# Kernel tuning notes

Measured on AMD Instinct MI355X. Metric: run time of the kernel, lower is better.

The kernel has to match this reference:

```python
import jax, jax.numpy as jnp
import numpy as np

EMBED_DIM = 2048
NUM_HEADS = 16
HEAD_DIM = EMBED_DIM // NUM_HEADS
BASE = 10000.0


def rotate_half(x):
    half = x.shape[-1] // 2
    x1, x2 = x[..., :half], x[..., half:]
    return jnp.concatenate([-x2, x1], axis=-1)


def apply_rope(x, base=BASE):
    # x: [B, H, S, Dh]
    S, Dh = x.shape[-2], x.shape[-1]
    inv_freq = 1.0 / (base ** (jnp.arange(0, Dh, 2, dtype=jnp.float32) / Dh))
    t = jnp.arange(S, dtype=jnp.float32)
    freqs = jnp.einsum('i,j->ij', t, inv_freq)          # [S, Dh/2]
    emb = jnp.concatenate([freqs, freqs], axis=-1)      # [S, Dh]
    return x * jnp.cos(emb) + rotate_half(x) * jnp.sin(emb)


def setup_inputs() -> dict:
    key = jax.random.key(0)
    ks = jax.random.split(key, 9)
    B, S, D = 2, 2048, EMBED_DIM
    xavier = lambda k, shape: jax.random.uniform(
        k, shape, jnp.float32, -1.0, 1.0) * float(np.sqrt(6.0 / (shape[0] + shape[1])))
    return {
        'x': jax.random.normal(ks[0], (B, S, D), jnp.float32),
        'q_w': xavier(ks[1], (D, D)),
        'k_w': xavier(ks[2], (D, D)),
        'v_w': xavier(ks[3], (D, D)),
        'q_b': jnp.zeros((D,), jnp.float32),
        'k_b': jnp.zeros((D,), jnp.float32),
        'v_b': jnp.zeros((D,), jnp.float32),
        'out_w': xavier(ks[4], (D, D)),
        'out_b': jnp.zeros((D,), jnp.float32),
    }


def reference(x, q_w, k_w, v_w, q_b, k_b, v_b, out_w, out_b):
    B, S, D = x.shape
    H, Dh = NUM_HEADS, HEAD_DIM
    scaling = Dh ** -0.5
    # F.linear(x, W, b) = x @ W.T + b
    q = (x @ q_w.T + q_b).reshape(B, S, H, Dh).transpose(0, 2, 1, 3)
    k = (x @ k_w.T + k_b).reshape(B, S, H, Dh).transpose(0, 2, 1, 3)
    v = (x @ v_w.T + v_b).reshape(B, S, H, Dh).transpose(0, 2, 1, 3)
    q = apply_rope(q)
    k = apply_rope(k)
    attn = jnp.einsum('bhqd,bhkd->bhqk', q, k) * scaling
    probs = jax.nn.softmax(attn, axis=-1)
    out = jnp.einsum('bhqk,bhkd->bhqd', probs, v)
    out = out.transpose(0, 2, 1, 3).reshape(B, S, D)
    return out @ out_w.T + out_b
```

## Files before the change

### kernel.cpp

```cpp
#include <hip/hip_runtime.h>
#include <stdint.h>

typedef __bf16 bf16;
typedef __bf16 bf16x4 __attribute__((ext_vector_type(4)));
typedef __bf16 bf16x8 __attribute__((ext_vector_type(8)));
typedef float f32x4 __attribute__((ext_vector_type(4)));

#define DM 2048
#define MM 4096
#define MFMA16(a, b, c) __builtin_amdgcn_mfma_f32_16x16x32_bf16(a, b, c, 0, 0, 0)

__device__ __forceinline__ void gload_lds16(const void* g, void* l) {
  __builtin_amdgcn_global_load_lds((const __attribute__((address_space(1))) uint32_t*)g,
                                   (__attribute__((address_space(3))) uint32_t*)l, 16, 0, 0);
}

__global__ __launch_bounds__(256) void cvt_f32_bf16(
    const float* __restrict__ s0, const float* __restrict__ s1,
    const float* __restrict__ s2, const float* __restrict__ s3,
    const float* __restrict__ s4,
    bf16* __restrict__ d0, bf16* __restrict__ d1, bf16* __restrict__ d2,
    bf16* __restrict__ d3, bf16* __restrict__ d4)
{
  const size_t i4 = (size_t)(blockIdx.x * 256 + threadIdx.x) * 4;
  const float* s; bf16* d; size_t off;
  if      (i4 <  8388608u) { s = s0; d = d0; off = i4;             }
  else if (i4 < 12582912u) { s = s1; d = d1; off = i4 -  8388608u; }
  else if (i4 < 16777216u) { s = s2; d = d2; off = i4 - 12582912u; }
  else if (i4 < 20971520u) { s = s3; d = d3; off = i4 - 16777216u; }
  else                     { s = s4; d = d4; off = i4 - 20971520u; }
  const float4 v = *(const float4*)(s + off);
  bf16x4 o = { (bf16)v.x, (bf16)v.y, (bf16)v.z, (bf16)v.w };
  *(bf16x4*)(d + off) = o;
}

__global__ __launch_bounds__(256, 2) void gemm_qkv_fused(
    const bf16* __restrict__ A,
    const bf16* __restrict__ Wq, const bf16* __restrict__ Wk, const bf16* __restrict__ Wv,
    const float* __restrict__ qb, const float* __restrict__ kb, const float* __restrict__ vb,
    bf16* __restrict__ Cq, bf16* __restrict__ Ck, bf16* __restrict__ Cv)
{
  __shared__ __align__(16) bf16 As[128 * 32];
  __shared__ __align__(16) bf16 Ws[3 * 128 * 32];
  const int id = blockIdx.x;
  const int xcd = id & 7, jj = id >> 3;
  const int n0 = (xcd * 2 + (jj >> 5)) * 128;
  const int m0 = (jj & 31) * 128;

  const int t = threadIdx.x;
  const int wave = t >> 6, lane = t & 63;
  const int quad = lane >> 4, c16 = lane & 15;
  const int wr = wave >> 1, wc = wave & 1;

  f32x4 acc[3][4][4] = {};

  const int rowA = t >> 2;
  const int colA = (t & 3) * 8;
  const bf16* gA  = A  + (size_t)(m0 + rowA) * DM + colA;
  const bf16* gW0 = Wq + (size_t)(n0 + rowA) * DM + colA;
  const bf16* gW1 = Wk + (size_t)(n0 + rowA) * DM + colA;
  const bf16* gW2 = Wv + (size_t)(n0 + rowA) * DM + colA;
  bf16* lA  = As + wave * 512;
  bf16* lW0 = Ws + wave * 512;
  bf16* lW1 = Ws + 4096 + wave * 512;
  bf16* lW2 = Ws + 8192 + wave * 512;

  for (int k0 = 0; k0 < DM; k0 += 32) {
    gload_lds16(gA,  lA);
    gload_lds16(gA  + (size_t)64 * DM, lA  + 2048);
    gload_lds16(gW0, lW0);
    gload_lds16(gW0 + (size_t)64 * DM, lW0 + 2048);
    gload_lds16(gW1, lW1);
    gload_lds16(gW1 + (size_t)64 * DM, lW1 + 2048);
    gload_lds16(gW2, lW2);
    gload_lds16(gW2 + (size_t)64 * DM, lW2 + 2048);
    gA += 32; gW0 += 32; gW1 += 32; gW2 += 32;
    __syncthreads();

    bf16x8 af[4];
#pragma unroll
    for (int i = 0; i < 4; ++i)
      af[i] = *(const bf16x8*)&As[(wr * 64 + i * 16 + c16) * 32 + quad * 8];
#pragma unroll
    for (int z = 0; z < 3; ++z) {
      bf16x8 bfr[4];
#pragma unroll
      for (int jx = 0; jx < 4; ++jx)
        bfr[jx] = *(const bf16x8*)&Ws[z * 4096 + (wc * 64 + jx * 16 + c16) * 32 + quad * 8];
#pragma unroll
      for (int i = 0; i < 4; ++i)
#pragma unroll
        for (int jx = 0; jx < 4; ++jx)
          acc[z][i][jx] = MFMA16(af[i], bfr[jx], acc[z][i][jx]);
    }
    __syncthreads();
  }

#pragma unroll
  for (int z = 0; z < 2; ++z) {
    bf16* C = (z == 0) ? Cq : Ck;
    const float* bias = (z == 0) ? qb : kb;
#pragma unroll
    for (int jx = 0; jx < 4; ++jx) {
      const int col = n0 + wc * 64 + jx * 16 + c16;
      const float bv = bias[col];
#pragma unroll
      for (int i = 0; i < 4; ++i) {
        const int row = m0 + wr * 64 + i * 16 + quad * 4;
#pragma unroll
        for (int r = 0; r < 4; ++r)
          C[(size_t)(row + r) * DM + col] = (bf16)(acc[z][i][jx][r] + bv);
      }
    }
  }
  {
    const int h = n0 >> 7;
#pragma unroll
    for (int jx = 0; jx < 4; ++jx) {
      const int d = wc * 64 + jx * 16 + c16;
      const float bv = vb[n0 + d];
#pragma unroll
      for (int i = 0; i < 4; ++i) {
        const int row = m0 + wr * 64 + i * 16 + quad * 4;
        const int b = row >> 11, s = row & 2047;
        bf16x4 o;
#pragma unroll
        for (int r = 0; r < 4; ++r) o[r] = (bf16)(acc[2][i][jx][r] + bv);
        *(bf16x4*)&Cv[((size_t)((b * 16 + h) * 128 + d)) * 2048 + s] = o;
      }
    }
  }
}

__global__ __launch_bounds__(256) void gemm_bias_f32(
    const bf16* __restrict__ A, const bf16* __restrict__ W,
    const float* __restrict__ bias, float* __restrict__ C)
{
  __shared__ __align__(16) bf16 As[128 * 32];
  __shared__ __align__(16) bf16 Bs[128 * 32];
  const int id = blockIdx.x;
  const int xcd = id & 7, jj = id >> 3;
  const int n0 = (xcd * 2 + (jj >> 5)) * 128;
  const int m0 = (jj & 31) * 128;

  const int t = threadIdx.x;
  const int wave = t >> 6, lane = t & 63;
  const int quad = lane >> 4, c16 = lane & 15;
  const int wr = wave >> 1, wc = wave & 1;

  f32x4 acc[4][4] = {};
  const int rowA = t >> 2;
  const int colA = (t & 3) * 8;
  const bf16* gA = A + (size_t)(m0 + rowA) * DM + colA;
  const bf16* gB = W + (size_t)(n0 + rowA) * DM + colA;
  bf16* lA = As + wave * 512;
  bf16* lB = Bs + wave * 512;

  for (int k0 = 0; k0 < DM; k0 += 32) {
    gload_lds16(gA, lA);
    gload_lds16(gA + (size_t)64 * DM, lA + 2048);
    gload_lds16(gB, lB);
    gload_lds16(gB + (size_t)64 * DM, lB + 2048);
    gA += 32; gB += 32;
    __syncthreads();

    bf16x8 af[4], bfr[4];
#pragma unroll
    for (int i = 0; i < 4; ++i)
      af[i] = *(const bf16x8*)&As[(wr * 64 + i * 16 + c16) * 32 + quad * 8];
#pragma unroll
    for (int jx = 0; jx < 4; ++jx)
      bfr[jx] = *(const bf16x8*)&Bs[(wc * 64 + jx * 16 + c16) * 32 + quad * 8];
#pragma unroll
    for (int i = 0; i < 4; ++i)
#pragma unroll
      for (int jx = 0; jx < 4; ++jx)
        acc[i][jx] = MFMA16(af[i], bfr[jx], acc[i][jx]);
    __syncthreads();
  }

#pragma unroll
  for (int jx = 0; jx < 4; ++jx) {
    const int col = n0 + wc * 64 + jx * 16 + c16;
    const float bv = bias[col];
#pragma unroll
    for (int i = 0; i < 4; ++i) {
      const int row = m0 + wr * 64 + i * 16 + quad * 4;
#pragma unroll
      for (int r = 0; r < 4; ++r)
        C[(size_t)(row + r) * DM + col] = acc[i][jx][r] + bv;
    }
  }
}

__global__ __launch_bounds__(256) void rope_scale(bf16* __restrict__ Q, bf16* __restrict__ K)
{
  const int idx = blockIdx.x * 256 + threadIdx.x;
  const int i = idx & 63;
  const int h = (idx >> 6) & 15;
  const int s = (idx >> 10) & 2047;
  const int b = idx >> 21;
  const size_t base = ((size_t)(b * 2048 + s)) * 2048 + (size_t)h * 128;
  const float inv_freq = __expf((float)i * -0.14391156514261228f);
  float sn, cs;
  __sincosf((float)s * inv_freq, &sn, &cs);
  const float scale = 0.08838834764831845f * 1.4426950408889634f;
  const float q1 = (float)Q[base + i], q2 = (float)Q[base + i + 64];
  Q[base + i]      = (bf16)((q1 * cs - q2 * sn) * scale);
  Q[base + i + 64] = (bf16)((q2 * cs + q1 * sn) * scale);
  const float k1 = (float)K[base + i], k2 = (float)K[base + i + 64];
  K[base + i]      = (bf16)(k1 * cs - k2 * sn);
  K[base + i + 64] = (bf16)(k2 * cs + k1 * sn);
}

__global__ __launch_bounds__(256, 2) void attn(
    const bf16* __restrict__ Q, const bf16* __restrict__ K,
    const bf16* __restrict__ Vt, bf16* __restrict__ O)
{
  __shared__ __align__(16) bf16 Ks[4][64][32];
  __shared__ __align__(16) bf16 Vs[2][128][32];
  __shared__ __align__(16) bf16 Ps[4][2][16][88];
  const int t = threadIdx.x;
  const int wave = t >> 6, lane = t & 63;
  const int quad = lane >> 4, c16 = lane & 15;
  const int id = blockIdx.x;
  const int xcd = id & 7, jj = id >> 3;
  const int bh = xcd * 4 + (jj >> 4);
  const int q0 = (jj & 15) * 128;
  const int b = bh >> 4, h = bh & 15;

  bf16x8 qf[2][4];
#pragma unroll
  for (int g = 0; g < 2; ++g) {
    const bf16* qrow = Q + (size_t)(b * 2048 + q0 + wave * 32 + g * 16 + c16) * 2048
                         + (size_t)h * 128 + quad * 8;
#pragma unroll
    for (int ks = 0; ks < 4; ++ks) qf[g][ks] = *(const bf16x8*)(qrow + ks * 32);
  }

  float l_i[2] = {0.f, 0.f};
  f32x4 o_acc[2][8] = {};

  const bf16* Kg = K + (size_t)(b * 2048) * 2048 + (size_t)h * 128;
  const bf16* Vg = Vt + (size_t)bh * 128 * 2048;

  for (int kt = 0; kt < 32; ++kt) {
    const int kt0 = kt * 64;
#pragma unroll
    for (int rr = 0; rr < 4; ++rr) {
      const int s = rr * 256 + t;
      const int ks = s >> 8, krow = (s >> 2) & 63, c8 = s & 3;
      gload_lds16(Kg + (size_t)(kt0 + krow) * 2048 + ks * 32 + c8 * 8,
                  (bf16*)Ks + (size_t)(rr * 256 + wave * 64) * 8);
    }
#pragma unroll
    for (int rr = 0; rr < 4; ++rr) {
      const int s = rr * 256 + t;
      const int kc = s >> 9, d = (s >> 2) & 127, c8 = s & 3;
      gload_lds16(Vg + (size_t)d * 2048 + kt0 + kc * 32 + c8 * 8,
                  (bf16*)Vs + (size_t)(rr * 256 + wave * 64) * 8);
    }
    __syncthreads();

    f32x4 st[2][4] = {};
#pragma unroll
    for (int ks = 0; ks < 4; ++ks)
#pragma unroll
      for (int nt = 0; nt < 4; ++nt) {
        bf16x8 kf = *(const bf16x8*)&Ks[ks][nt * 16 + c16][quad * 8];
        st[0][nt] = MFMA16(kf, qf[0][ks], st[0][nt]);
        st[1][nt] = MFMA16(kf, qf[1][ks], st[1][nt]);
      }

#pragma unroll
    for (int g = 0; g < 2; ++g) {
      float ps = 0.f;
#pragma unroll
      for (int nt = 0; nt < 4; ++nt) {
        bf16x4 pk;
#pragma unroll
        for (int r = 0; r < 4; ++r) {
          const float p = exp2f(st[g][nt][r]);
          ps += p;
          pk[r] = (bf16)p;
        }
        *(bf16x4*)&Ps[wave][g][c16][nt * 16 + quad * 4] = pk;
      }
      l_i[g] += ps;
    }

#pragma unroll
    for (int kc = 0; kc < 2; ++kc) {
      bf16x8 pf0 = *(const bf16x8*)&Ps[wave][0][c16][kc * 32 + quad * 8];
      bf16x8 pf1 = *(const bf16x8*)&Ps[wave][1][c16][kc * 32 + quad * 8];
#pragma unroll
      for (int dt = 0; dt < 8; ++dt) {
        bf16x8 vf = *(const bf16x8*)&Vs[kc][dt * 16 + c16][quad * 8];
        o_acc[0][dt] = MFMA16(vf, pf0, o_acc[0][dt]);
        o_acc[1][dt] = MFMA16(vf, pf1, o_acc[1][dt]);
      }
    }
    __syncthreads();
  }

#pragma unroll
  for (int g = 0; g < 2; ++g) {
    float l = l_i[g];
    l += __shfl_xor(l, 16, 64);
    l += __shfl_xor(l, 32, 64);
    const float invl = 1.0f / l;
    const int qrow = q0 + wave * 32 + g * 16 + c16;
    bf16* orow = O + (size_t)(b * 2048 + qrow) * 2048 + (size_t)h * 128 + quad * 4;
#pragma unroll
    for (int dt = 0; dt < 8; ++dt) {
      bf16x4 o;
#pragma unroll
      for (int r = 0; r < 4; ++r) o[r] = (bf16)(o_acc[g][dt][r] * invl);
      *(bf16x4*)(orow + dt * 16) = o;
    }
  }
}

extern "C" void kernel_launch(void* const* d_in, const int* in_sizes, int n_in,
                              void* d_out, int out_size, void* d_ws, size_t ws_size,
                              hipStream_t stream)
{
  (void)in_sizes; (void)n_in; (void)out_size; (void)ws_size;
  const float* x   = (const float*)d_in[0];
  const float* q_w = (const float*)d_in[1];
  const float* k_w = (const float*)d_in[2];
  const float* v_w = (const float*)d_in[3];
  const float* q_b = (const float*)d_in[4];
  const float* k_b = (const float*)d_in[5];
  const float* v_b = (const float*)d_in[6];
  const float* o_w = (const float*)d_in[7];
  const float* o_b = (const float*)d_in[8];

  const size_t NELEM = (size_t)MM * DM;
  const size_t WELEM = (size_t)DM * DM;
  bf16* Xb  = (bf16*)d_ws;
  bf16* Wq  = Xb + NELEM;
  bf16* Wk  = Wq + WELEM;
  bf16* Wv  = Wk + WELEM;
  bf16* Wo  = Wv + WELEM;
  bf16* Q   = Wo + WELEM;
  bf16* Kb  = Q  + NELEM;
  bf16* Vt  = Kb + NELEM;
  bf16* attnO = Xb;

  cvt_f32_bf16<<<24576, 256, 0, stream>>>(x, q_w, k_w, v_w, o_w, Xb, Wq, Wk, Wv, Wo);

  gemm_qkv_fused<<<512, 256, 0, stream>>>(Xb, Wq, Wk, Wv, q_b, k_b, v_b, Q, Kb, Vt);
  rope_scale<<<16384, 256, 0, stream>>>(Q, Kb);
  attn<<<512, 256, 0, stream>>>(Q, Kb, Vt, attnO);
  gemm_bias_f32<<<512, 256, 0, stream>>>(attnO, Wo, o_b, (float*)d_out);
}
```

Measured before the change: 410.8 us.

## Fuse RoPE into QKV GEMM epilogue, widen K-tile with XOR-swizzled LDS

Removes the separate rope_scale kernel and applies rotary embedding plus softmax scaling inside the QKV GEMM epilogue. The epilogue stages each Q/K tile through LDS so it can write coalesced 16-byte rows. Both GEMMs now load 64-wide K tiles into an XOR-swizzled LDS layout, which halves the barrier count and avoids bank conflicts. The attention kernel's launch bounds go to 3 blocks per CU with a smaller P padding, and the output GEMM gets a 2-block occupancy hint. The QKV kernel now uses 64KB of LDS, which may cut its occupancy.

```diff
diff --git a/kernel.cpp b/kernel.cpp
--- a/kernel.cpp
+++ b/kernel.cpp
@@ -40,8 +40,10 @@
     const float* __restrict__ qb, const float* __restrict__ kb, const float* __restrict__ vb,
     bf16* __restrict__ Cq, bf16* __restrict__ Ck, bf16* __restrict__ Cv)
 {
-  __shared__ __align__(16) bf16 As[128 * 32];
-  __shared__ __align__(16) bf16 Ws[3 * 128 * 32];
+  __shared__ __align__(16) bf16 smem[32768];
+  bf16* As = smem;
+  bf16* Ws = smem + 8192;
+
   const int id = blockIdx.x;
   const int xcd = id & 7, jj = id >> 3;
   const int n0 = (xcd * 2 + (jj >> 5)) * 128;
@@ -54,90 +56,118 @@
 
   f32x4 acc[3][4][4] = {};
 
-  const int rowA = t >> 2;
-  const int colA = (t & 3) * 8;
-  const bf16* gA  = A  + (size_t)(m0 + rowA) * DM + colA;
-  const bf16* gW0 = Wq + (size_t)(n0 + rowA) * DM + colA;
-  const bf16* gW1 = Wk + (size_t)(n0 + rowA) * DM + colA;
-  const bf16* gW2 = Wv + (size_t)(n0 + rowA) * DM + colA;
-  bf16* lA  = As + wave * 512;
-  bf16* lW0 = Ws + wave * 512;
-  bf16* lW1 = Ws + 4096 + wave * 512;
-  bf16* lW2 = Ws + 8192 + wave * 512;
-
-  for (int k0 = 0; k0 < DM; k0 += 32) {
-    gload_lds16(gA,  lA);
-    gload_lds16(gA  + (size_t)64 * DM, lA  + 2048);
-    gload_lds16(gW0, lW0);
-    gload_lds16(gW0 + (size_t)64 * DM, lW0 + 2048);
-    gload_lds16(gW1, lW1);
-    gload_lds16(gW1 + (size_t)64 * DM, lW1 + 2048);
-    gload_lds16(gW2, lW2);
-    gload_lds16(gW2 + (size_t)64 * DM, lW2 + 2048);
-    gA += 32; gW0 += 32; gW1 += 32; gW2 += 32;
-    __syncthreads();
-
-    bf16x8 af[4];
-#pragma unroll
-    for (int i = 0; i < 4; ++i)
-      af[i] = *(const bf16x8*)&As[(wr * 64 + i * 16 + c16) * 32 + quad * 8];
-#pragma unroll
-    for (int z = 0; z < 3; ++z) {
-      bf16x8 bfr[4];
-#pragma unroll
-      for (int jx = 0; jx < 4; ++jx)
-        bfr[jx] = *(const bf16x8*)&Ws[z * 4096 + (wc * 64 + jx * 16 + c16) * 32 + quad * 8];
-#pragma unroll
-      for (int i = 0; i < 4; ++i)
-#pragma unroll
-        for (int jx = 0; jx < 4; ++jx)
-          acc[z][i][jx] = MFMA16(af[i], bfr[jx], acc[z][i][jx]);
-    }
-    __syncthreads();
-  }
-
+  const int srow = t >> 3;
+  const int scol = ((t & 7) ^ (srow & 7)) * 8;
+  const bf16* gA  = A  + (size_t)(m0 + srow) * DM + scol;
+  const bf16* gW0 = Wq + (size_t)(n0 + srow) * DM + scol;
+  const bf16* gW1 = Wk + (size_t)(n0 + srow) * DM + scol;
+  const bf16* gW2 = Wv + (size_t)(n0 + srow) * DM + scol;
+
+  for (int k0 = 0; k0 < DM; k0 += 64) {
+#pragma unroll
+    for (int rr = 0; rr < 4; ++rr) {
+      const size_t go = (size_t)(rr * 32) * DM;
+      const int lo = (rr * 256 + wave * 64) * 8;
+      gload_lds16(gA  + go, As + lo);
+      gload_lds16(gW0 + go, Ws + lo);
+      gload_lds16(gW1 + go, Ws + 8192 + lo);
+      gload_lds16(gW2 + go, Ws + 16384 + lo);
+    }
+    gA += 64; gW0 += 64; gW1 += 64; gW2 += 64;
+    __syncthreads();
+
+#pragma unroll
+    for (int ks = 0; ks < 2; ++ks) {
+      bf16x8 af[4];
+#pragma unroll
+      for (int i = 0; i < 4; ++i) {
+        const int row = wr * 64 + i * 16 + c16;
+        const int gi = (ks * 4 + quad) ^ (row & 7);
+        af[i] = *(const bf16x8*)&As[row * 64 + gi * 8];
+      }
+#pragma unroll
+      for (int z = 0; z < 3; ++z) {
+        bf16x8 bfr[4];
+#pragma unroll
+        for (int jx = 0; jx < 4; ++jx) {
+          const int row = wc * 64 + jx * 16 + c16;
+          const int gi = (ks * 4 + quad) ^ (row & 7);
+          bfr[jx] = *(const bf16x8*)&Ws[z * 8192 + row * 64 + gi * 8];
+        }
+#pragma unroll
+        for (int i = 0; i < 4; ++i)
+#pragma unroll
+          for (int jx = 0; jx < 4; ++jx)
+            acc[z][i][jx] = MFMA16(af[i], bfr[jx], acc[z][i][jx]);
+      }
+    }
+    __syncthreads();
+  }
+
+  const int h = n0 >> 7;
+#pragma unroll
+  for (int jx = 0; jx < 4; ++jx) {
+    const int d = wc * 64 + jx * 16 + c16;
+    const float bv = vb[n0 + d];
+#pragma unroll
+    for (int i = 0; i < 4; ++i) {
+      const int row = m0 + wr * 64 + i * 16 + quad * 4;
+      const int b = row >> 11, s = row & 2047;
+      bf16x4 o;
+#pragma unroll
+      for (int r = 0; r < 4; ++r) o[r] = (bf16)(acc[2][i][jx][r] + bv);
+      *(bf16x4*)&Cv[((size_t)((b * 16 + h) * 128 + d)) * 2048 + s] = o;
+    }
+  }
+
+  bf16* Tl = smem;
 #pragma unroll
   for (int z = 0; z < 2; ++z) {
+    __syncthreads();
+#pragma unroll
+    for (int jx = 0; jx < 4; ++jx) {
+      const int col = wc * 64 + jx * 16 + c16;
+      const float bv = (z == 0 ? qb : kb)[n0 + col];
+#pragma unroll
+      for (int i = 0; i < 4; ++i) {
+        const int row = wr * 64 + i * 16 + quad * 4;
+#pragma unroll
+        for (int r = 0; r < 4; ++r)
+          Tl[(row + r) * 136 + col] = (bf16)(acc[z][i][jx][r] + bv);
+      }
+    }
+    __syncthreads();
     bf16* C = (z == 0) ? Cq : Ck;
-    const float* bias = (z == 0) ? qb : kb;
-#pragma unroll
-    for (int jx = 0; jx < 4; ++jx) {
-      const int col = n0 + wc * 64 + jx * 16 + c16;
-      const float bv = bias[col];
-#pragma unroll
-      for (int i = 0; i < 4; ++i) {
-        const int row = m0 + wr * 64 + i * 16 + quad * 4;
-#pragma unroll
-        for (int r = 0; r < 4; ++r)
-          C[(size_t)(row + r) * DM + col] = (bf16)(acc[z][i][jx][r] + bv);
-      }
-    }
-  }
-  {
-    const int h = n0 >> 7;
-#pragma unroll
-    for (int jx = 0; jx < 4; ++jx) {
-      const int d = wc * 64 + jx * 16 + c16;
-      const float bv = vb[n0 + d];
-#pragma unroll
-      for (int i = 0; i < 4; ++i) {
-        const int row = m0 + wr * 64 + i * 16 + quad * 4;
-        const int b = row >> 11, s = row & 2047;
-        bf16x4 o;
-#pragma unroll
-        for (int r = 0; r < 4; ++r) o[r] = (bf16)(acc[2][i][jx][r] + bv);
-        *(bf16x4*)&Cv[((size_t)((b * 16 + h) * 128 + d)) * 2048 + s] = o;
-      }
-    }
-  }
-}
-
-__global__ __launch_bounds__(256) void gemm_bias_f32(
+    const float scale = (z == 0) ? 0.08838834764831845f * 1.4426950408889634f : 1.0f;
+#pragma unroll
+    for (int rr = 0; rr < 4; ++rr) {
+      const int row = rr * 32 + (t >> 3);
+      const int d0 = (t & 7) * 8;
+      const int s = (m0 + row) & 2047;
+      bf16x8 xa = *(const bf16x8*)&Tl[row * 136 + d0];
+      bf16x8 xb = *(const bf16x8*)&Tl[row * 136 + d0 + 64];
+      bf16x8 o1, o2;
+#pragma unroll
+      for (int j = 0; j < 8; ++j) {
+        const float inv_freq = __expf((float)(d0 + j) * -0.14391156514261228f);
+        float sn, cs;
+        __sincosf((float)s * inv_freq, &sn, &cs);
+        const float a = (float)xa[j], bb = (float)xb[j];
+        o1[j] = (bf16)((a * cs - bb * sn) * scale);
+        o2[j] = (bf16)((bb * cs + a * sn) * scale);
+      }
+      *(bf16x8*)&C[(size_t)(m0 + row) * DM + n0 + d0]      = o1;
+      *(bf16x8*)&C[(size_t)(m0 + row) * DM + n0 + d0 + 64] = o2;
+    }
+  }
+}
+
+__global__ __launch_bounds__(256, 2) void gemm_bias_f32(
     const bf16* __restrict__ A, const bf16* __restrict__ W,
     const float* __restrict__ bias, float* __restrict__ C)
 {
-  __shared__ __align__(16) bf16 As[128 * 32];
-  __shared__ __align__(16) bf16 Bs[128 * 32];
+  __shared__ __align__(16) bf16 As[8192];
+  __shared__ __align__(16) bf16 Bs[8192];
   const int id = blockIdx.x;
   const int xcd = id & 7, jj = id >> 3;
   const int n0 = (xcd * 2 + (jj >> 5)) * 128;
@@ -149,33 +179,43 @@
   const int wr = wave >> 1, wc = wave & 1;
 
   f32x4 acc[4][4] = {};
-  const int rowA = t >> 2;
-  const int colA = (t & 3) * 8;
-  const bf16* gA = A + (size_t)(m0 + rowA) * DM + colA;
-  const bf16* gB = W + (size_t)(n0 + rowA) * DM + colA;
-  bf16* lA = As + wave * 512;
-  bf16* lB = Bs + wave * 512;
-
-  for (int k0 = 0; k0 < DM; k0 += 32) {
-    gload_lds16(gA, lA);
-    gload_lds16(gA + (size_t)64 * DM, lA + 2048);
-    gload_lds16(gB, lB);
-    gload_lds16(gB + (size_t)64 * DM, lB + 2048);
-    gA += 32; gB += 32;
-    __syncthreads();
-
-    bf16x8 af[4], bfr[4];
-#pragma unroll
-    for (int i = 0; i < 4; ++i)
-      af[i] = *(const bf16x8*)&As[(wr * 64 + i * 16 + c16) * 32 + quad * 8];
-#pragma unroll
-    for (int jx = 0; jx < 4; ++jx)
-      bfr[jx] = *(const bf16x8*)&Bs[(wc * 64 + jx * 16 + c16) * 32 + quad * 8];
-#pragma unroll
-    for (int i = 0; i < 4; ++i)
-#pragma unroll
-      for (int jx = 0; jx < 4; ++jx)
-        acc[i][jx] = MFMA16(af[i], bfr[jx], acc[i][jx]);
+  const int srow = t >> 3;
+  const int scol = ((t & 7) ^ (srow & 7)) * 8;
+  const bf16* gA = A + (size_t)(m0 + srow) * DM + scol;
+  const bf16* gB = W + (size_t)(n0 + srow) * DM + scol;
+
+  for (int k0 = 0; k0 < DM; k0 += 64) {
+#pragma unroll
+    for (int rr = 0; rr < 4; ++rr) {
+      const size_t go = (size_t)(rr * 32) * DM;
+      const int lo = (rr * 256 + wave * 64) * 8;
+      gload_lds16(gA + go, As + lo);
+      gload_lds16(gB + go, Bs + lo);
+    }
+    gA += 64; gB += 64;
+    __syncthreads();
+
+#pragma unroll
+    for (int ks = 0; ks < 2; ++ks) {
+      bf16x8 af[4], bfr[4];
+#pragma unroll
+      for (int i = 0; i < 4; ++i) {
+        const int row = wr * 64 + i * 16 + c16;
+        const int gi = (ks * 4 + quad) ^ (row & 7);
+        af[i] = *(const bf16x8*)&As[row * 64 + gi * 8];
+      }
+#pragma unroll
+      for (int jx = 0; jx < 4; ++jx) {
+        const int row = wc * 64 + jx * 16 + c16;
+        const int gi = (ks * 4 + quad) ^ (row & 7);
+        bfr[jx] = *(const bf16x8*)&Bs[row * 64 + gi * 8];
+      }
+#pragma unroll
+      for (int i = 0; i < 4; ++i)
+#pragma unroll
+        for (int jx = 0; jx < 4; ++jx)
+          acc[i][jx] = MFMA16(af[i], bfr[jx], acc[i][jx]);
+    }
     __syncthreads();
   }
 
@@ -193,33 +233,13 @@
   }
 }
 
-__global__ __launch_bounds__(256) void rope_scale(bf16* __restrict__ Q, bf16* __restrict__ K)
-{
-  const int idx = blockIdx.x * 256 + threadIdx.x;
-  const int i = idx & 63;
-  const int h = (idx >> 6) & 15;
-  const int s = (idx >> 10) & 2047;
-  const int b = idx >> 21;
-  const size_t base = ((size_t)(b * 2048 + s)) * 2048 + (size_t)h * 128;
-  const float inv_freq = __expf((float)i * -0.14391156514261228f);
-  float sn, cs;
-  __sincosf((float)s * inv_freq, &sn, &cs);
-  const float scale = 0.08838834764831845f * 1.4426950408889634f;
-  const float q1 = (float)Q[base + i], q2 = (float)Q[base + i + 64];
-  Q[base + i]      = (bf16)((q1 * cs - q2 * sn) * scale);
-  Q[base + i + 64] = (bf16)((q2 * cs + q1 * sn) * scale);
-  const float k1 = (float)K[base + i], k2 = (float)K[base + i + 64];
-  K[base + i]      = (bf16)(k1 * cs - k2 * sn);
-  K[base + i + 64] = (bf16)(k2 * cs + k1 * sn);
-}
-
-__global__ __launch_bounds__(256, 2) void attn(
+__global__ __launch_bounds__(256, 3) void attn(
     const bf16* __restrict__ Q, const bf16* __restrict__ K,
     const bf16* __restrict__ Vt, bf16* __restrict__ O)
 {
   __shared__ __align__(16) bf16 Ks[4][64][32];
   __shared__ __align__(16) bf16 Vs[2][128][32];
-  __shared__ __align__(16) bf16 Ps[4][2][16][88];
+  __shared__ __align__(16) bf16 Ps[4][2][16][80];
   const int t = threadIdx.x;
   const int wave = t >> 6, lane = t & 63;
   const int quad = lane >> 4, c16 = lane & 15;
@@ -351,7 +371,6 @@
   cvt_f32_bf16<<<24576, 256, 0, stream>>>(x, q_w, k_w, v_w, o_w, Xb, Wq, Wk, Wv, Wo);
 
   gemm_qkv_fused<<<512, 256, 0, stream>>>(Xb, Wq, Wk, Wv, q_b, k_b, v_b, Q, Kb, Vt);
-  rope_scale<<<16384, 256, 0, stream>>>(Q, Kb);
   attn<<<512, 256, 0, stream>>>(Q, Kb, Vt, attnO);
   gemm_bias_f32<<<512, 256, 0, stream>>>(attnO, Wo, o_b, (float*)d_out);
 }
```

After: 393.9 us. -4.1%, faster.
